# Optimization experiments

Hardware: AMD Instinct MI355X
Metric: run time of the kernel (lower is better)

The kernel has to match this reference:

```python
import jax, jax.numpy as jnp
import numpy as np

SIGMA2 = 1.9 * 1.9   # LJ sigma^2 (Angstrom^2)
EPS = 0.2            # LJ well depth
R2_SOFT = 0.25       # softening to keep energies finite for random dofs


def _local_ht(dofs):
    """dofs [..., 9] -> local homogeneous transform [..., 4, 4].
    Uses (phi, theta, d) bond-style dofs: R = Rz(phi) @ Ry(theta),
    translation d along the rotated x-axis."""
    phi, theta = dofs[..., 0], dofs[..., 1]
    d = 1.5 + 0.25 * jnp.tanh(dofs[..., 2])  # bond length ~1.25..1.75 A
    cp, sp = jnp.cos(phi), jnp.sin(phi)
    ct, st = jnp.cos(theta), jnp.sin(theta)
    r00, r01, r02 = cp * ct, -sp, cp * st
    r10, r11, r12 = sp * ct, cp, sp * st
    r20, r21, r22 = -st, jnp.zeros_like(ct), ct
    tx, ty, tz = d * r00, d * r10, d * r20
    zero, one = jnp.zeros_like(phi), jnp.ones_like(phi)
    ht = jnp.stack([
        jnp.stack([r00, r01, r02, tx], -1),
        jnp.stack([r10, r11, r12, ty], -1),
        jnp.stack([r20, r21, r22, tz], -1),
        jnp.stack([zero, zero, zero, one], -1),
    ], -2)
    return ht


def _forward_kin(full_dofs, P, A):
    # per-pose chain kinforest: cumulative left-product of local HTs
    ht = _local_ht(full_dofs.reshape(P, A, 9))  # [P, A, 4, 4]
    compose = lambda a, b: jnp.einsum('...ij,...jk->...ik', a, b)
    cum = jax.lax.associative_scan(compose, ht, axis=1)
    return cum[..., :3, 3].reshape(-1, 3)  # [P*A, 3]


def _lj_score(coords):
    # coords [P, A, 3] -> per-pose softened LJ energy [P]
    sq = jnp.sum(coords * coords, axis=-1)                 # [P, A]
    G = jnp.einsum('pad,pbd->pab', coords, coords)         # [P, A, A] GEMM
    r2 = sq[:, :, None] + sq[:, None, :] - 2.0 * G + R2_SOFT
    inv6 = (SIGMA2 / r2) ** 3
    e = 4.0 * EPS * (inv6 * inv6 - inv6)
    A = coords.shape[1]
    mask = jnp.triu(jnp.ones((A, A), dtype=coords.dtype), k=1)  # i < j
    return jnp.sum(e * mask, axis=(1, 2))


def setup_inputs() -> dict:
    key = jax.random.key(0)
    k1, k2 = jax.random.split(key)
    P, A = 4, 4096
    full_dofs = 0.5 * jax.random.normal(k1, (P * A, 9), dtype=jnp.float32)
    pose_stack_coords = 5.0 * jax.random.normal(k2, (P, A, 3), dtype=jnp.float32)
    kinforest_id = jnp.arange(P * A, dtype=jnp.int64)
    return {"full_dofs": full_dofs, "pose_stack_coords": pose_stack_coords,
            "kinforest_id": kinforest_id}


def reference(full_dofs, pose_stack_coords, kinforest_id):
    P, A, _ = pose_stack_coords.shape
    kincoords = _forward_kin(full_dofs, P, A)  # [P*A, 3]
    coords = pose_stack_coords.reshape(-1, 3).at[kinforest_id].set(kincoords)
    coords = coords.reshape(P, A, 3)
    return _lj_score(coords)  # [P]
```

## Files before the change

### kernel.cpp

```cpp
#include <hip/hip_runtime.h>
#include <math.h>

#define A_ATOMS 4096
#define P_POSES 4
#define N_TOT   (A_ATOMS * P_POSES)
#define TILE    128
#define NTILES  (A_ATOMS / TILE)
#define JG      8
#define NJG     (NTILES / JG)
#define NSTRIPS 80
#define LJ_T    512

#define SEG     64
#define NSEG    (A_ATOMS / SEG)
#define APPLY_T 256
#define APPLY_B (A_ATOMS / APPLY_T)

typedef float v2f __attribute__((ext_vector_type(2)));

__device__ __constant__ float c_SIGMA2  = 1.9f * 1.9f;
__device__ __constant__ float c_4EPS    = 0.8f;
__device__ __constant__ float c_R2SOFT  = 0.25f;

struct RT { float m[12]; };

__device__ inline RT rt_identity() {
    RT v;
    v.m[0]=1.f; v.m[1]=0.f; v.m[2]=0.f;  v.m[3]=0.f;
    v.m[4]=0.f; v.m[5]=1.f; v.m[6]=0.f;  v.m[7]=0.f;
    v.m[8]=0.f; v.m[9]=0.f; v.m[10]=1.f; v.m[11]=0.f;
    return v;
}

__device__ inline RT rt_compose(const RT& a, const RT& b) {
    RT c;
#pragma unroll
    for (int i = 0; i < 3; ++i) {
        float a0 = a.m[i*4+0], a1 = a.m[i*4+1], a2 = a.m[i*4+2];
        c.m[i*4+0] = fmaf(a0, b.m[0], fmaf(a1, b.m[4],  a2*b.m[8]));
        c.m[i*4+1] = fmaf(a0, b.m[1], fmaf(a1, b.m[5],  a2*b.m[9]));
        c.m[i*4+2] = fmaf(a0, b.m[2], fmaf(a1, b.m[6],  a2*b.m[10]));
        c.m[i*4+3] = fmaf(a0, b.m[3], fmaf(a1, b.m[7],  fmaf(a2, b.m[11], a.m[i*4+3])));
    }
    return c;
}

__device__ inline RT rt_shfl_up(const RT& a, int off) {
    RT r;
#pragma unroll
    for (int i = 0; i < 12; ++i) r.m[i] = __shfl_up(a.m[i], off, 64);
    return r;
}

__device__ inline RT local_ht(const float* __restrict__ dof) {
    float phi = dof[0], th = dof[1];
    float d = fmaf(0.25f, tanhf(dof[2]), 1.5f);
    float sp, cp, st, ct;
    sincosf(phi, &sp, &cp);
    sincosf(th,  &st, &ct);
    RT h;
    h.m[0] = cp*ct; h.m[1] = -sp; h.m[2]  = cp*st; h.m[3]  = d*cp*ct;
    h.m[4] = sp*ct; h.m[5] =  cp; h.m[6]  = sp*st; h.m[7]  = d*sp*ct;
    h.m[8] = -st;   h.m[9] = 0.f; h.m[10] = ct;    h.m[11] = -d*st;
    return h;
}

__global__ __launch_bounds__(SEG) void fk_scan(const float* __restrict__ dofs,
                                               float* __restrict__ Tx,
                                               float* __restrict__ Ty,
                                               float* __restrict__ Tz,
                                               float4* __restrict__ S0,
                                               float4* __restrict__ S1,
                                               float4* __restrict__ S2) {
    const int pose = blockIdx.x >> 6;
    const int seg  = blockIdx.x & (NSEG - 1);
    const int lane = threadIdx.x;
    const int g    = pose * A_ATOMS + seg * SEG + lane;

    RT v = local_ht(dofs + (size_t)g * 9);

#pragma unroll
    for (int off = 1; off < 64; off <<= 1) {
        RT l = rt_shfl_up(v, off);
        if (lane >= off) v = rt_compose(l, v);
    }

    Tx[g] = v.m[3]; Ty[g] = v.m[7]; Tz[g] = v.m[11];

    if (lane == 63) {
        int s = pose * NSEG + seg;
        S0[s] = make_float4(v.m[0], v.m[1], v.m[2],  v.m[3]);
        S1[s] = make_float4(v.m[4], v.m[5], v.m[6],  v.m[7]);
        S2[s] = make_float4(v.m[8], v.m[9], v.m[10], v.m[11]);
    }
}

__global__ __launch_bounds__(APPLY_T) void fk_apply(const int* __restrict__ kid,
                                                    const float* __restrict__ Tx,
                                                    const float* __restrict__ Ty,
                                                    const float* __restrict__ Tz,
                                                    const float4* __restrict__ S0,
                                                    const float4* __restrict__ S1,
                                                    const float4* __restrict__ S2,
                                                    float4* __restrict__ C4,
                                                    float* __restrict__ out) {
    __shared__ float4 e0[NSEG], e1[NSEG], e2[NSEG];

    const int pose = blockIdx.y;
    const int blk  = blockIdx.x;
    const int tid  = threadIdx.x;
    if (blk == 0 && tid == 0) out[pose] = 0.f;

    if (tid < 64) {
        int s = pose * NSEG + tid;
        float4 a0 = S0[s], a1 = S1[s], a2 = S2[s];
        RT v;
        v.m[0]=a0.x; v.m[1]=a0.y; v.m[2]=a0.z;  v.m[3]=a0.w;
        v.m[4]=a1.x; v.m[5]=a1.y; v.m[6]=a1.z;  v.m[7]=a1.w;
        v.m[8]=a2.x; v.m[9]=a2.y; v.m[10]=a2.z; v.m[11]=a2.w;
#pragma unroll
        for (int off = 1; off < 64; off <<= 1) {
            RT l = rt_shfl_up(v, off);
            if (tid >= off) v = rt_compose(l, v);
        }
        RT ex = rt_shfl_up(v, 1);
        if (tid == 0) ex = rt_identity();
        e0[tid] = make_float4(ex.m[0], ex.m[1], ex.m[2],  ex.m[3]);
        e1[tid] = make_float4(ex.m[4], ex.m[5], ex.m[6],  ex.m[7]);
        e2[tid] = make_float4(ex.m[8], ex.m[9], ex.m[10], ex.m[11]);
    }
    __syncthreads();

    const int a = blk * APPLY_T + tid;
    const int g = pose * A_ATOMS + a;
    float rx = Tx[g], ry = Ty[g], rz = Tz[g];
    float4 x0 = e0[a >> 6], x1 = e1[a >> 6], x2 = e2[a >> 6];
    float tx = fmaf(x0.x, rx, fmaf(x0.y, ry, fmaf(x0.z, rz, x0.w)));
    float ty = fmaf(x1.x, rx, fmaf(x1.y, ry, fmaf(x1.z, rz, x1.w)));
    float tz = fmaf(x2.x, rx, fmaf(x2.y, ry, fmaf(x2.z, rz, x2.w)));
    C4[kid[g]] = make_float4(tx, ty, tz, 0.f);
}

__global__ __launch_bounds__(LJ_T) void lj_kernel(const float4* __restrict__ C4,
                                                  float* __restrict__ out) {
    const int pose = blockIdx.y;
    int rr = blockIdx.x, bi = 0;
    while (rr >= NJG - (bi >> 3)) { rr -= NJG - (bi >> 3); ++bi; }
    const int jg = (bi >> 3) + rr;
    const int t0 = (jg == (bi >> 3)) ? (bi & 7) : 0;

    __shared__ float sxi[TILE], syi[TILE], szi[TILE];
    __shared__ float sxj[2][TILE], syj[2][TILE], szj[2][TILE];

    const int tid = threadIdx.x;
    const float4* Cp = C4 + pose * A_ATOMS;

    if (tid < TILE) {
        float4 c = Cp[bi * TILE + tid];
        sxi[tid] = c.x; syi[tid] = c.y; szi[tid] = c.z;
    } else if (tid < 2 * TILE) {
        int t = tid - TILE;
        float4 c = Cp[(jg * JG + t0) * TILE + t];
        sxj[0][t] = c.x; syj[0][t] = c.y; szj[0][t] = c.z;
    }
    __syncthreads();

    const int i0 = (tid & 31) * 4;
    const int j0 = (tid >> 5) * 8;

    const float SIG2 = c_SIGMA2, SOFT = c_R2SOFT;

    float xi[4], yi[4], zi[4];
#pragma unroll
    for (int k = 0; k < 4; ++k) {
        xi[k] = sxi[i0 + k]; yi[k] = syi[i0 + k]; zi[k] = szi[i0 + k];
    }

    float acc = 0.f;
    int cur = 0;

    for (int t = t0; t < JG; ++t) {
        const int bj = jg * JG + t;

        float4 p4;
        const bool pf = (t < JG - 1) && (tid >= 3 * TILE);
        if (pf) p4 = Cp[(bj + 1) * TILE + (tid - 3 * TILE)];

        if (bi != bj) {
            v2f xj2[4], yj2[4], zj2[4];
#pragma unroll
            for (int p = 0; p < 4; ++p) {
                xj2[p] = (v2f){sxj[cur][j0 + 2*p], sxj[cur][j0 + 2*p + 1]};
                yj2[p] = (v2f){syj[cur][j0 + 2*p], syj[cur][j0 + 2*p + 1]};
                zj2[p] = (v2f){szj[cur][j0 + 2*p], szj[cur][j0 + 2*p + 1]};
            }
            const v2f soft2 = (v2f){SOFT, SOFT};
            v2f acc2 = (v2f){0.f, 0.f};
#pragma unroll
            for (int p = 0; p < 4; ++p) {
#pragma unroll
                for (int k = 0; k < 4; ++k) {
                    v2f dx = xi[k] - xj2[p];
                    v2f dy = yi[k] - yj2[p];
                    v2f dz = zi[k] - zj2[p];
                    v2f r2 = __builtin_elementwise_fma(dx, dx,
                             __builtin_elementwise_fma(dy, dy,
                             __builtin_elementwise_fma(dz, dz, soft2)));
                    v2f rc = (v2f){__builtin_amdgcn_rcpf(r2.x), __builtin_amdgcn_rcpf(r2.y)};
                    v2f tt = SIG2 * rc;
                    v2f i6 = tt * tt * tt;
                    acc2 += __builtin_elementwise_fma(i6, i6, -i6);
                }
            }
            acc += acc2.x + acc2.y;
        } else {
            float xj[8], yj[8], zj[8];
#pragma unroll
            for (int k = 0; k < 8; ++k) {
                xj[k] = sxj[cur][j0 + k]; yj[k] = syj[cur][j0 + k]; zj[k] = szj[cur][j0 + k];
            }
#pragma unroll
            for (int jj = 0; jj < 8; ++jj) {
                int j = j0 + jj;
#pragma unroll
                for (int k = 0; k < 4; ++k) {
                    float dx = xi[k] - xj[jj], dy = yi[k] - yj[jj], dz = zi[k] - zj[jj];
                    float r2 = fmaf(dx, dx, fmaf(dy, dy, fmaf(dz, dz, SOFT)));
                    float tt = SIG2 * __builtin_amdgcn_rcpf(r2);
                    float i6 = tt * tt * tt;
                    float hh = fmaf(i6, i6, -i6);
                    acc += ((i0 + k) < j) ? hh : 0.f;
                }
            }
        }

        if (t < JG - 1) {
            if (pf) {
                int tl = tid - 3 * TILE;
                sxj[1 - cur][tl] = p4.x; syj[1 - cur][tl] = p4.y; szj[1 - cur][tl] = p4.z;
            }
            __syncthreads();
            cur ^= 1;
        }
    }
    acc *= c_4EPS;

#pragma unroll
    for (int off = 32; off > 0; off >>= 1) acc += __shfl_down(acc, off, 64);

    __shared__ float wsum[LJ_T / 64];
    int lane = tid & 63, wid = tid >> 6;
    if (lane == 0) wsum[wid] = acc;
    __syncthreads();
    if (tid == 0) {
        float s = 0.f;
#pragma unroll
        for (int w = 0; w < LJ_T / 64; ++w) s += wsum[w];
        atomicAdd(out + pose, s);
    }
}

extern "C" void kernel_launch(void* const* d_in, const int* in_sizes, int n_in,
                              void* d_out, int out_size, void* d_ws, size_t ws_size,
                              hipStream_t stream) {
    (void)in_sizes; (void)n_in; (void)out_size; (void)ws_size;
    const float* dofs = (const float*)d_in[0];
    const int*   kid  = (const int*)d_in[2];
    float*       out  = (float*)d_out;

    float4* C4 = (float4*)d_ws;
    float*  Tx = (float*)(C4 + N_TOT);
    float*  Ty = Tx + N_TOT;
    float*  Tz = Ty + N_TOT;
    float4* S0 = (float4*)(Tz + N_TOT);
    float4* S1 = S0 + P_POSES * NSEG;
    float4* S2 = S1 + P_POSES * NSEG;

    fk_scan<<<P_POSES * NSEG, SEG, 0, stream>>>(dofs, Tx, Ty, Tz, S0, S1, S2);
    dim3 agrid(APPLY_B, P_POSES);
    fk_apply<<<agrid, APPLY_T, 0, stream>>>(kid, Tx, Ty, Tz, S0, S1, S2, C4, out);
    dim3 grid(NSTRIPS, P_POSES);
    lj_kernel<<<grid, LJ_T, 0, stream>>>(C4, out);
}
```

Measured before the change: 79.77 us.

## Restructure LJ kernel to one wave per 64x64 segment pair

Replaces the strip-based 128x128 tile LJ kernel with a flat grid where each wavefront handles one upper-triangular 64x64 segment pair, one i-atom per lane and j-atoms broadcast from LDS. This aims to give finer-grained, better-balanced work across CUs and higher occupancy, and it removes the double-buffered prefetch loop. In exchange it loses per-thread register reuse of i-coordinates, adds more LDS reads per pair, and adds more blocks and atomics.

Measured after the change: 79.60 us. Within noise of the previous version (-0.2%).

```diff
diff --git a/kernel.cpp b/kernel.cpp
--- a/kernel.cpp
+++ b/kernel.cpp
@@ -4,17 +4,17 @@
 #define A_ATOMS 4096
 #define P_POSES 4
 #define N_TOT   (A_ATOMS * P_POSES)
-#define TILE    128
-#define NTILES  (A_ATOMS / TILE)
-#define JG      8
-#define NJG     (NTILES / JG)
-#define NSTRIPS 80
-#define LJ_T    512
 
 #define SEG     64
 #define NSEG    (A_ATOMS / SEG)
 #define APPLY_T 256
 #define APPLY_B (A_ATOMS / APPLY_T)
+
+#define SEGP_PER_POSE (NSEG * (NSEG + 1) / 2)
+#define SEGP_TOT      (SEGP_PER_POSE * P_POSES)
+#define LJW_T   512
+#define WPB     (LJW_T / 64)
+#define LJ_BLOCKS (SEGP_TOT / WPB)
 
 typedef float v2f __attribute__((ext_vector_type(2)));
 
@@ -141,121 +141,86 @@
     C4[kid[g]] = make_float4(tx, ty, tz, 0.f);
 }
 
-__global__ __launch_bounds__(LJ_T) void lj_kernel(const float4* __restrict__ C4,
-                                                  float* __restrict__ out) {
-    const int pose = blockIdx.y;
-    int rr = blockIdx.x, bi = 0;
-    while (rr >= NJG - (bi >> 3)) { rr -= NJG - (bi >> 3); ++bi; }
-    const int jg = (bi >> 3) + rr;
-    const int t0 = (jg == (bi >> 3)) ? (bi & 7) : 0;
-
-    __shared__ float sxi[TILE], syi[TILE], szi[TILE];
-    __shared__ float sxj[2][TILE], syj[2][TILE], szj[2][TILE];
-
-    const int tid = threadIdx.x;
+__global__ __launch_bounds__(LJW_T, 4) void lj_kernel(const float4* __restrict__ C4,
+                                                      float* __restrict__ out) {
+    __shared__ float4 jb[WPB][SEG];
+    __shared__ float  wsum[WPB];
+
+    const int tid  = threadIdx.x;
+    const int lane = tid & 63;
+    const int wid  = tid >> 6;
+
+    const int spi  = __builtin_amdgcn_readfirstlane(blockIdx.x * WPB + wid);
+    const int pose = spi / SEGP_PER_POSE;
+    int r  = spi - pose * SEGP_PER_POSE;
+    int si = 0;
+    while (r >= NSEG - si) { r -= NSEG - si; ++si; }
+    const int sj = si + r;
+
     const float4* Cp = C4 + pose * A_ATOMS;
-
-    if (tid < TILE) {
-        float4 c = Cp[bi * TILE + tid];
-        sxi[tid] = c.x; syi[tid] = c.y; szi[tid] = c.z;
-    } else if (tid < 2 * TILE) {
-        int t = tid - TILE;
-        float4 c = Cp[(jg * JG + t0) * TILE + t];
-        sxj[0][t] = c.x; syj[0][t] = c.y; szj[0][t] = c.z;
-    }
+    float4 ci = Cp[si * SEG + lane];
+    jb[wid][lane] = Cp[sj * SEG + lane];
     __syncthreads();
 
-    const int i0 = (tid & 31) * 4;
-    const int j0 = (tid >> 5) * 8;
-
     const float SIG2 = c_SIGMA2, SOFT = c_R2SOFT;
-
-    float xi[4], yi[4], zi[4];
-#pragma unroll
-    for (int k = 0; k < 4; ++k) {
-        xi[k] = sxi[i0 + k]; yi[k] = syi[i0 + k]; zi[k] = szi[i0 + k];
-    }
-
+    const float xi = ci.x, yi = ci.y, zi = ci.z;
     float acc = 0.f;
-    int cur = 0;
-
-    for (int t = t0; t < JG; ++t) {
-        const int bj = jg * JG + t;
-
-        float4 p4;
-        const bool pf = (t < JG - 1) && (tid >= 3 * TILE);
-        if (pf) p4 = Cp[(bj + 1) * TILE + (tid - 3 * TILE)];
-
-        if (bi != bj) {
-            v2f xj2[4], yj2[4], zj2[4];
-#pragma unroll
-            for (int p = 0; p < 4; ++p) {
-                xj2[p] = (v2f){sxj[cur][j0 + 2*p], sxj[cur][j0 + 2*p + 1]};
-                yj2[p] = (v2f){syj[cur][j0 + 2*p], syj[cur][j0 + 2*p + 1]};
-                zj2[p] = (v2f){szj[cur][j0 + 2*p], szj[cur][j0 + 2*p + 1]};
+
+    if (si != sj) {
+        const v2f soft2 = (v2f){SOFT, SOFT};
+        v2f acc2 = (v2f){0.f, 0.f};
+#pragma unroll
+        for (int q = 0; q < SEG; q += 4) {
+            float4 a = jb[wid][q + 0];
+            float4 b = jb[wid][q + 1];
+            float4 c = jb[wid][q + 2];
+            float4 d = jb[wid][q + 3];
+            {
+                v2f xj = (v2f){a.x, b.x}, yj = (v2f){a.y, b.y}, zj = (v2f){a.z, b.z};
+                v2f dx = xi - xj, dy = yi - yj, dz = zi - zj;
+                v2f r2 = __builtin_elementwise_fma(dx, dx,
+                         __builtin_elementwise_fma(dy, dy,
+                         __builtin_elementwise_fma(dz, dz, soft2)));
+                v2f rc = (v2f){__builtin_amdgcn_rcpf(r2.x), __builtin_amdgcn_rcpf(r2.y)};
+                v2f tt = SIG2 * rc;
+                v2f i6 = tt * tt * tt;
+                acc2 += __builtin_elementwise_fma(i6, i6, -i6);
             }
-            const v2f soft2 = (v2f){SOFT, SOFT};
-            v2f acc2 = (v2f){0.f, 0.f};
-#pragma unroll
-            for (int p = 0; p < 4; ++p) {
-#pragma unroll
-                for (int k = 0; k < 4; ++k) {
-                    v2f dx = xi[k] - xj2[p];
-                    v2f dy = yi[k] - yj2[p];
-                    v2f dz = zi[k] - zj2[p];
-                    v2f r2 = __builtin_elementwise_fma(dx, dx,
-                             __builtin_elementwise_fma(dy, dy,
-                             __builtin_elementwise_fma(dz, dz, soft2)));
-                    v2f rc = (v2f){__builtin_amdgcn_rcpf(r2.x), __builtin_amdgcn_rcpf(r2.y)};
-                    v2f tt = SIG2 * rc;
-                    v2f i6 = tt * tt * tt;
-                    acc2 += __builtin_elementwise_fma(i6, i6, -i6);
-                }
-            }
-            acc += acc2.x + acc2.y;
-        } else {
-            float xj[8], yj[8], zj[8];
-#pragma unroll
-            for (int k = 0; k < 8; ++k) {
-                xj[k] = sxj[cur][j0 + k]; yj[k] = syj[cur][j0 + k]; zj[k] = szj[cur][j0 + k];
-            }
-#pragma unroll
-            for (int jj = 0; jj < 8; ++jj) {
-                int j = j0 + jj;
-#pragma unroll
-                for (int k = 0; k < 4; ++k) {
-                    float dx = xi[k] - xj[jj], dy = yi[k] - yj[jj], dz = zi[k] - zj[jj];
-                    float r2 = fmaf(dx, dx, fmaf(dy, dy, fmaf(dz, dz, SOFT)));
-                    float tt = SIG2 * __builtin_amdgcn_rcpf(r2);
-                    float i6 = tt * tt * tt;
-                    float hh = fmaf(i6, i6, -i6);
-                    acc += ((i0 + k) < j) ? hh : 0.f;
-                }
+            {
+                v2f xj = (v2f){c.x, d.x}, yj = (v2f){c.y, d.y}, zj = (v2f){c.z, d.z};
+                v2f dx = xi - xj, dy = yi - yj, dz = zi - zj;
+                v2f r2 = __builtin_elementwise_fma(dx, dx,
+                         __builtin_elementwise_fma(dy, dy,
+                         __builtin_elementwise_fma(dz, dz, soft2)));
+                v2f rc = (v2f){__builtin_amdgcn_rcpf(r2.x), __builtin_amdgcn_rcpf(r2.y)};
+                v2f tt = SIG2 * rc;
+                v2f i6 = tt * tt * tt;
+                acc2 += __builtin_elementwise_fma(i6, i6, -i6);
             }
         }
-
-        if (t < JG - 1) {
-            if (pf) {
-                int tl = tid - 3 * TILE;
-                sxj[1 - cur][tl] = p4.x; syj[1 - cur][tl] = p4.y; szj[1 - cur][tl] = p4.z;
-            }
-            __syncthreads();
-            cur ^= 1;
+        acc = acc2.x + acc2.y;
+    } else {
+#pragma unroll 8
+        for (int q = 0; q < SEG; ++q) {
+            float4 a = jb[wid][q];
+            float dx = xi - a.x, dy = yi - a.y, dz = zi - a.z;
+            float r2 = fmaf(dx, dx, fmaf(dy, dy, fmaf(dz, dz, SOFT)));
+            float tt = SIG2 * __builtin_amdgcn_rcpf(r2);
+            float i6 = tt * tt * tt;
+            float hh = fmaf(i6, i6, -i6);
+            acc += (lane < q) ? hh : 0.f;
         }
     }
     acc *= c_4EPS;
 
 #pragma unroll
     for (int off = 32; off > 0; off >>= 1) acc += __shfl_down(acc, off, 64);
-
-    __shared__ float wsum[LJ_T / 64];
-    int lane = tid & 63, wid = tid >> 6;
     if (lane == 0) wsum[wid] = acc;
     __syncthreads();
     if (tid == 0) {
         float s = 0.f;
 #pragma unroll
-        for (int w = 0; w < LJ_T / 64; ++w) s += wsum[w];
+        for (int w = 0; w < WPB; ++w) s += wsum[w];
         atomicAdd(out + pose, s);
     }
 }
@@ -279,6 +244,5 @@
     fk_scan<<<P_POSES * NSEG, SEG, 0, stream>>>(dofs, Tx, Ty, Tz, S0, S1, S2);
     dim3 agrid(APPLY_B, P_POSES);
     fk_apply<<<agrid, APPLY_T, 0, stream>>>(kid, Tx, Ty, Tz, S0, S1, S2, C4, out);
-    dim3 grid(NSTRIPS, P_POSES);
-    lj_kernel<<<grid, LJ_T, 0, stream>>>(C4, out);
-}
+    lj_kernel<<<LJ_BLOCKS, LJW_T, 0, stream>>>(C4, out);
+}
```
